# Optimization experiments

Measured on AMD Instinct MI355X. Metric: run time of the kernel, lower is better.

The kernel has to match this reference:

```python
import jax, jax.numpy as jnp
import numpy as np

N, E, F, H, L, G, EMB, C = 50000, 600000, 128, 128, 4, 64, 64, 10
BN_EPS = 1e-5


def setup_inputs() -> dict:
    key = jax.random.key(0)
    k = lambda i: jax.random.fold_in(key, i)
    s = 0.05  # weight scale
    return {
        "x": jax.random.normal(k(0), (N, F), jnp.float32),
        "edge_index": jax.random.randint(k(1), (2, E), 0, N, jnp.int64),
        "batch": jnp.sort(jax.random.randint(k(2), (N,), 0, G, jnp.int64)),
        "emb": jax.random.normal(k(3), (G, EMB), jnp.float32),
        "eps": jnp.zeros((L,), jnp.float32),
        "W1": jax.random.normal(k(4), (L, F, H), jnp.float32) * s,
        "b1": jnp.zeros((L, H), jnp.float32),
        "W2": jax.random.normal(k(5), (L, H, H), jnp.float32) * s,
        "b2": jnp.zeros((L, H), jnp.float32),
        "gamma": jnp.ones((L, H), jnp.float32),
        "beta": jnp.zeros((L, H), jnp.float32),
        "lin1_w": jax.random.normal(k(6), (L * H + EMB, 2 * H), jnp.float32) * s,
        "lin1_b": jnp.zeros((2 * H,), jnp.float32),
        "lin2_w": jax.random.normal(k(7), (2 * H, H), jnp.float32) * s,
        "lin2_b": jnp.zeros((H,), jnp.float32),
        "lin4_w": jax.random.normal(k(8), (H, C), jnp.float32) * s,
        "lin4_b": jnp.zeros((C,), jnp.float32),
    }


def _gin_mlp(h, W1, b1, W2, b2, gamma, beta):
    # Linear -> ReLU -> Linear -> ReLU -> BatchNorm1d (batch stats)
    h = jax.nn.relu(h @ W1 + b1)
    h = jax.nn.relu(h @ W2 + b2)
    mean = jnp.mean(h, axis=0)
    var = jnp.var(h, axis=0)
    return (h - mean) * jax.lax.rsqrt(var + BN_EPS) * gamma + beta


def reference(x, edge_index, batch, emb, eps, W1, b1, W2, b2, gamma, beta,
              lin1_w, lin1_b, lin2_w, lin2_b, lin4_w, lin4_b):
    src, dst = edge_index[0], edge_index[1]
    xs = []
    for l in range(L):
        # GIN: MLP((1+eps)*x_i + sum_{j->i} x_j)  via gather + scatter-add
        agg = jax.ops.segment_sum(x[src], dst, num_segments=N)  # [N,H]
        x = _gin_mlp((1.0 + eps[l]) * x + agg,
                     W1[l], b1[l], W2[l], b2[l], gamma[l], beta[l])
        xs.append(x)
    h = jnp.concatenate(xs, axis=1)  # [N, L*H]
    # global mean pool per graph
    sums = jax.ops.segment_sum(h, batch, num_segments=G)  # [G, L*H]
    cnt = jax.ops.segment_sum(jnp.ones((N,), h.dtype), batch, num_segments=G)
    pooled = sums / jnp.maximum(cnt, 1.0)[:, None]
    z = jnp.concatenate([pooled, emb.reshape(G, -1)], axis=1)
    z = jax.nn.relu(z @ lin1_w + lin1_b)  # .relu() twice is idempotent
    # dropout p=0.5 skipped (eval mode); lin3 unused in original forward
    z = jax.nn.relu(z @ lin2_w + lin2_b)
    z = z @ lin4_w + lin4_b
    return jax.nn.log_softmax(z, axis=1)
```

## Files before the change

### kernel.cpp

```cpp
#include <hip/hip_runtime.h>
#include <cstdint>
#include <cstddef>

#define N_NODES 50000
#define N_EDGES 600000
#define NLAYER  4
#define NGRAPH  64
#define SCAN_NB 196
#define NBLK_MLP ((N_NODES + 127) / 128)
#define CVTX_NB ((N_NODES * 32 + 255) / 256)
#define CVTW_NB ((NLAYER * 128 * 128 * 2) / 256)
#define DEG_NB  ((N_EDGES + 255) / 256)

typedef unsigned int   u32;
typedef unsigned short u16;
typedef unsigned char  u8;
typedef float f32x4  __attribute__((ext_vector_type(4)));
typedef short bf16x8 __attribute__((ext_vector_type(8)));

__device__ __forceinline__ u16 f2bf(float f) {
    u32 x = __float_as_uint(f);
    u32 r = x + 0x7fffu + ((x >> 16) & 1u);
    return (u16)(r >> 16);
}
__device__ __forceinline__ u32 pack2(float a, float b) {
    return (u32)f2bf(a) | ((u32)f2bf(b) << 16);
}

__device__ __forceinline__ float fp8b0(u32 u) { return __builtin_amdgcn_cvt_f32_fp8(u, 0); }
__device__ __forceinline__ float fp8b1(u32 u) { return __builtin_amdgcn_cvt_f32_fp8(u, 1); }
__device__ __forceinline__ u32 pk_fp8(float a, float b) {
    return (u32)__builtin_amdgcn_cvt_pk_fp8_f32(a, b, 0, false);
}

__global__ __launch_bounds__(256) void setup_all(
    const float4* __restrict__ x, u32* __restrict__ xf8,
    const float* __restrict__ W1, const float* __restrict__ W2,
    short* __restrict__ W1t, short* __restrict__ W2t,
    const int* __restrict__ dst, int* __restrict__ deg) {
    int b = blockIdx.x, tid = threadIdx.x;
    if (b < CVTX_NB) {
        int i = b * 256 + tid;
        if (i < N_NODES * 32) {
            float4 v = x[i];
            u32 r = pk_fp8(v.x, v.y);
            r = (u32)__builtin_amdgcn_cvt_pk_fp8_f32(v.z, v.w, (int)r, true);
            xf8[i] = r;
        }
    } else if (b < CVTX_NB + CVTW_NB) {
        int i = (b - CVTX_NB) * 256 + tid;
        int z = i >> 16, r = i & 65535;
        int l = r >> 14, n = (r >> 7) & 127, k = r & 127;
        const float* W = z ? W2 : W1;
        short* Wt      = z ? W2t : W1t;
        Wt[((size_t)l * 128 + n) * 128 + k] = (short)f2bf(W[((size_t)l * 128 + k) * 128 + n]);
    } else {
        int e = (b - CVTX_NB - CVTW_NB) * 256 + tid;
        if (e < N_EDGES) atomicAdd(&deg[dst[e]], 1);
    }
}

__global__ __launch_bounds__(256) void scan_l1(const int* __restrict__ deg,
                                               int* __restrict__ bscan,
                                               int* __restrict__ bsum) {
    __shared__ int sd[256];
    int tid = threadIdx.x;
    int i = blockIdx.x * 256 + tid;
    int v = (i < N_NODES) ? deg[i] : 0;
    sd[tid] = v; __syncthreads();
#pragma unroll
    for (int off = 1; off < 256; off <<= 1) {
        int t = (tid >= off) ? sd[tid - off] : 0;
        __syncthreads();
        sd[tid] += t; __syncthreads();
    }
    if (i < N_NODES) bscan[i] = sd[tid];
    if (tid == 255) bsum[blockIdx.x] = sd[255];
}

__global__ __launch_bounds__(256) void scan_l3(const int* __restrict__ bscan,
                                               const int* __restrict__ bsum,
                                               int* __restrict__ rowp) {
    __shared__ int sd[256];
    __shared__ int sboff;
    int tid = threadIdx.x;
    int v = (tid < SCAN_NB) ? bsum[tid] : 0;
    sd[tid] = v; __syncthreads();
#pragma unroll
    for (int off = 1; off < 256; off <<= 1) {
        int t = (tid >= off) ? sd[tid - off] : 0;
        __syncthreads();
        sd[tid] += t; __syncthreads();
    }
    if (tid == (int)blockIdx.x) sboff = sd[tid] - v;
    __syncthreads();
    int i = blockIdx.x * 256 + tid;
    if (i == 0) rowp[0] = 0;
    if (i < N_NODES) rowp[i + 1] = bscan[i] + sboff;
}

__global__ void fill_csr(const int* __restrict__ src, const int* __restrict__ dst,
                         const int* __restrict__ rowp, int* __restrict__ cursor,
                         int* __restrict__ col) {
    int e = blockIdx.x * 256 + threadIdx.x;
    if (e < N_EDGES) {
        int d = dst[e];
        int pos = atomicAdd(&cursor[d], 1);
        col[rowp[d] + pos] = src[e];
    }
}

__global__ __launch_bounds__(256) void agg_kernel(
    const u16* __restrict__ xin,
    const float* __restrict__ sums_prev,
    const float* __restrict__ gamma, const float* __restrict__ beta,
    int layer, const float* __restrict__ eps_all,
    const int* __restrict__ rowp, const int* __restrict__ col,
    u32* __restrict__ agg) {
    __shared__ float cA[128], cD[128];
    int tid = threadIdx.x;
    if (tid < 128) {
        float a = 1.f, d = 0.f;
        if (sums_prev) {
            float s1 = sums_prev[tid], s2 = sums_prev[128 + tid];
            float mean = s1 * (1.0f / N_NODES);
            float var  = s2 * (1.0f / N_NODES) - mean * mean;
            a = rsqrtf(var + 1e-5f) * gamma[(layer - 1) * 128 + tid];
            d = beta[(layer - 1) * 128 + tid] - mean * a;
        }
        cA[tid] = a; cD[tid] = d;
    }
    __syncthreads();
    int node = blockIdx.x * 4 + (tid >> 6);
    int lane = tid & 63;
    if (node >= N_NODES) return;
    float a0 = cA[2 * lane], a1 = cA[2 * lane + 1];
    float d0 = cD[2 * lane], d1 = cD[2 * lane + 1];
    float ep = 1.0f + eps_all[layer];
    u32 v = xin[(size_t)node * 64 + lane];
    int k0 = rowp[node], k1 = rowp[node + 1];
    float s0 = 0.f, s1 = 0.f;
    int k = k0;
    int cc[8];
    if (k < k1) {
#pragma unroll
        for (int t = 0; t < 8; t++) cc[t] = col[min(k + t, k1 - 1)];
    }
    while (k < k1) {
        int idx[8];
#pragma unroll
        for (int t = 0; t < 8; t++) idx[t] = cc[t];
        int kn = k + 8;
        if (kn < k1) {
#pragma unroll
            for (int t = 0; t < 8; t++) cc[t] = col[min(kn + t, k1 - 1)];
        }
#pragma unroll
        for (int t = 0; t < 8; t++) {
            u32 u = xin[(size_t)idx[t] * 64 + lane];
            float w = (k + t < k1) ? 1.f : 0.f;
            s0 += w * fp8b0(u); s1 += w * fp8b1(u);
        }
        k = kn;
    }
    float deg = (float)(k1 - k0);
    float r0 = ep * (a0 * fp8b0(v) + d0) + a0 * s0 + deg * d0;
    float r1 = ep * (a1 * fp8b1(v) + d1) + a1 * s1 + deg * d1;
    agg[(size_t)node * 64 + lane] = pack2(r0, r1);
}

#define H1_STRIDE 136
__global__ __launch_bounds__(256) void mlp_fused(
    const short* __restrict__ A,
    const short* __restrict__ W1t, const float* __restrict__ b1,
    const short* __restrict__ W2t, const float* __restrict__ b2,
    u8* __restrict__ H2, const int* __restrict__ batch,
    float* __restrict__ sums, float* __restrict__ gsum, int M) {
    __shared__ alignas(16) short h1s[128 * H1_STRIDE];
    __shared__ int sh_ga, sh_gb, sh_split;
    int tid  = threadIdx.x;
    int wave = tid >> 6, lane = tid & 63;
    int ln15 = lane & 15, quad = lane >> 4;
    int m0blk = blockIdx.x * 128;
    int m0 = m0blk + wave * 32;
    const bf16x8 zz = {0, 0, 0, 0, 0, 0, 0, 0};

    if (tid == 0) {
        int rlo = m0blk, rhi = min(m0blk + 127, M - 1);
        int ga = batch[rlo], gb = batch[rhi];
        int split = m0blk + 128;
        if (ga != gb) {
            int lo = rlo, hi = rhi;
            while (lo + 1 < hi) { int mid = (lo + hi) >> 1; if (batch[mid] == ga) lo = mid; else hi = mid; }
            split = hi;
        }
        sh_ga = ga; sh_gb = gb; sh_split = split;
    }

    bf16x8 a[2][4];
#pragma unroll
    for (int rt = 0; rt < 2; rt++) {
        int row = m0 + rt * 16 + ln15;
        const short* rp = A + (size_t)row * 128 + quad * 8;
        bool ok = row < M;
#pragma unroll
        for (int s = 0; s < 4; s++)
            a[rt][s] = ok ? *(const bf16x8*)(rp + s * 32) : zz;
    }
#pragma unroll
    for (int ct = 0; ct < 8; ct++) {
        const short* wp = W1t + (size_t)(ct * 16 + ln15) * 128 + quad * 8;
        bf16x8 b[4];
#pragma unroll
        for (int s = 0; s < 4; s++) b[s] = *(const bf16x8*)(wp + s * 32);
        float bias = b1[ct * 16 + ln15];
#pragma unroll
        for (int rt = 0; rt < 2; rt++) {
            f32x4 acc = {0.f, 0.f, 0.f, 0.f};
#pragma unroll
            for (int s = 0; s < 4; s++)
                acc = __builtin_amdgcn_mfma_f32_16x16x32_bf16(a[rt][s], b[s], acc, 0, 0, 0);
#pragma unroll
            for (int i = 0; i < 4; i++) {
                float v = fmaxf(acc[i] + bias, 0.f);
                int lr = wave * 32 + rt * 16 + quad * 4 + i;
                h1s[lr * H1_STRIDE + ct * 16 + ln15] = (short)f2bf(v);
            }
        }
    }
    __syncthreads();
    bf16x8 c[2][4];
#pragma unroll
    for (int rt = 0; rt < 2; rt++) {
        const short* rp = h1s + (size_t)(wave * 32 + rt * 16 + ln15) * H1_STRIDE + quad * 8;
#pragma unroll
        for (int s = 0; s < 4; s++) c[rt][s] = *(const bf16x8*)(rp + s * 32);
    }
    int gsplit = sh_split;
    float sAcc[8], qAcc[8], pAcc[8];
#pragma unroll
    for (int ct = 0; ct < 8; ct++) { sAcc[ct] = 0.f; qAcc[ct] = 0.f; pAcc[ct] = 0.f; }
#pragma unroll
    for (int ct = 0; ct < 8; ct++) {
        const short* wp = W2t + (size_t)(ct * 16 + ln15) * 128 + quad * 8;
        bf16x8 b[4];
#pragma unroll
        for (int s = 0; s < 4; s++) b[s] = *(const bf16x8*)(wp + s * 32);
        float bias = b2[ct * 16 + ln15];
#pragma unroll
        for (int rt = 0; rt < 2; rt++) {
            f32x4 acc = {0.f, 0.f, 0.f, 0.f};
#pragma unroll
            for (int s = 0; s < 4; s++)
                acc = __builtin_amdgcn_mfma_f32_16x16x32_bf16(c[rt][s], b[s], acc, 0, 0, 0);
            int colx = ct * 16 + ln15;
#pragma unroll
            for (int i = 0; i < 4; i++) {
                int row = m0 + rt * 16 + quad * 4 + i;
                float v = fmaxf(acc[i] + bias, 0.f);
                if (row < M) H2[(size_t)row * 128 + colx] = (u8)(pk_fp8(v, v) & 0xffu);
                float vm = (row < M) ? v : 0.f;
                sAcc[ct] += vm; qAcc[ct] += vm * vm;
                if (row < gsplit) pAcc[ct] += vm;
            }
        }
    }
    __syncthreads();
    float* scr = (float*)h1s;
    int slice = wave * 4 + quad;
#pragma unroll
    for (int ct = 0; ct < 8; ct++) {
        int colx = ct * 16 + ln15;
        scr[(0 * 16 + slice) * 128 + colx] = sAcc[ct];
        scr[(1 * 16 + slice) * 128 + colx] = qAcc[ct];
        scr[(2 * 16 + slice) * 128 + colx] = pAcc[ct];
    }
    __syncthreads();
    if (tid < 128) {
        float ss = 0.f, qq = 0.f, pa = 0.f;
#pragma unroll
        for (int sl = 0; sl < 16; sl++) {
            ss += scr[(0 * 16 + sl) * 128 + tid];
            qq += scr[(1 * 16 + sl) * 128 + tid];
            pa += scr[(2 * 16 + sl) * 128 + tid];
        }
        atomicAdd(&sums[tid], ss);
        atomicAdd(&sums[128 + tid], qq);
        int ga = sh_ga, gb = sh_gb;
        atomicAdd(&gsum[ga * 128 + tid], pa);
        if (gb != ga) atomicAdd(&gsum[gb * 128 + tid], ss - pa);
    }
}

__global__ __launch_bounds__(256) void head_kernel(
    const float* __restrict__ gsum, const float* __restrict__ sumsL,
    const float* __restrict__ gamma, const float* __restrict__ beta,
    const int* __restrict__ batch, const float* __restrict__ emb,
    const float* __restrict__ l1w, const float* __restrict__ l1b,
    const float* __restrict__ l2w, const float* __restrict__ l2b,
    const float* __restrict__ l4w, const float* __restrict__ l4b,
    float* __restrict__ out) {
    __shared__ float z[576];
    __shared__ float z1[256];
    __shared__ float z2h[2][128];
    __shared__ float z2[128];
    __shared__ float zr[128][10];
    __shared__ float inv_cnt;
    int g = blockIdx.x;
    int tid = threadIdx.x;
    if (tid == 0) {
        int lo = 0, hi = N_NODES;
        while (lo < hi) { int m = (lo + hi) >> 1; if (batch[m] < g) lo = m + 1; else hi = m; }
        int s = lo;
        lo = 0; hi = N_NODES;
        while (lo < hi) { int m = (lo + hi) >> 1; if (batch[m] < g + 1) lo = m + 1; else hi = m; }
        inv_cnt = 1.0f / fmaxf((float)(lo - s), 1.0f);
    }
    __syncthreads();
    for (int j = tid; j < 512; j += 256) {
        int l = j >> 7, c = j & 127;
        float s1 = sumsL[l * 256 + c], s2 = sumsL[l * 256 + 128 + c];
        float mean = s1 * (1.0f / N_NODES);
        float var  = s2 * (1.0f / N_NODES) - mean * mean;
        float a = rsqrtf(var + 1e-5f) * gamma[l * 128 + c];
        float d = beta[l * 128 + c] - mean * a;
        z[j] = a * gsum[(size_t)l * NGRAPH * 128 + g * 128 + c] * inv_cnt + d;
    }
    if (tid < 64) z[512 + tid] = emb[g * 64 + tid];
    __syncthreads();
    {
        float acc = l1b[tid];
        for (int j0 = 0; j0 < 576; j0 += 16) {
            float lw[16];
#pragma unroll
            for (int t = 0; t < 16; t++) lw[t] = l1w[(j0 + t) * 256 + tid];
#pragma unroll
            for (int t = 0; t < 16; t++) acc += z[j0 + t] * lw[t];
        }
        z1[tid] = fmaxf(acc, 0.f);
    }
    __syncthreads();
    {
        int c2 = tid & 127, half = tid >> 7;
        float acc = 0.f;
        int jb = half * 128;
        for (int j0 = 0; j0 < 128; j0 += 8) {
            float lw[8];
#pragma unroll
            for (int t = 0; t < 8; t++) lw[t] = l2w[(jb + j0 + t) * 128 + c2];
#pragma unroll
            for (int t = 0; t < 8; t++) acc += z1[jb + j0 + t] * lw[t];
        }
        z2h[half][c2] = acc;
    }
    __syncthreads();
    if (tid < 128) z2[tid] = fmaxf(z2h[0][tid] + z2h[1][tid] + l2b[tid], 0.f);
    __syncthreads();
    if (tid < 128) {
        float zv = z2[tid];
        const float* wr = l4w + tid * 10;
#pragma unroll
        for (int c = 0; c < 10; c++) zr[tid][c] = zv * wr[c];
    }
    __syncthreads();
    for (int s = 64; s >= 1; s >>= 1) {
        if (tid < s) {
#pragma unroll
            for (int c = 0; c < 10; c++) zr[tid][c] += zr[tid + s][c];
        }
        __syncthreads();
    }
    if (tid == 0) {
        float z3s[10];
#pragma unroll
        for (int c = 0; c < 10; c++) z3s[c] = zr[0][c] + l4b[c];
        float m = z3s[0];
        for (int i = 1; i < 10; i++) m = fmaxf(m, z3s[i]);
        float se = 0.f;
        for (int i = 0; i < 10; i++) se += expf(z3s[i] - m);
        float lse = m + logf(se);
        for (int i = 0; i < 10; i++) out[g * 10 + i] = z3s[i] - lse;
    }
}

extern "C" void kernel_launch(void* const* d_in, const int* in_sizes, int n_in,
                              void* d_out, int out_size, void* d_ws, size_t ws_size,
                              hipStream_t stream) {
    (void)in_sizes; (void)n_in; (void)out_size; (void)ws_size;
    const float* x0   = (const float*)d_in[0];
    const int* ei     = (const int*)d_in[1];
    const int* src    = ei;
    const int* dst    = ei + N_EDGES;
    const int* batch  = (const int*)d_in[2];
    const float* emb  = (const float*)d_in[3];
    const float* eps  = (const float*)d_in[4];
    const float* W1   = (const float*)d_in[5];
    const float* b1   = (const float*)d_in[6];
    const float* W2   = (const float*)d_in[7];
    const float* b2   = (const float*)d_in[8];
    const float* gamma= (const float*)d_in[9];
    const float* beta = (const float*)d_in[10];
    const float* l1w  = (const float*)d_in[11];
    const float* l1b  = (const float*)d_in[12];
    const float* l2w  = (const float*)d_in[13];
    const float* l2b  = (const float*)d_in[14];
    const float* l4w  = (const float*)d_in[15];
    const float* l4b  = (const float*)d_in[16];

    char* ws = (char*)d_ws;
    size_t off = 0;
    auto alloc = [&](size_t bytes) -> char* {
        char* p = ws + off; off += (bytes + 255) & ~(size_t)255; return p;
    };
    int* deg    = (int*)alloc(N_NODES * 4);
    int* cursor = (int*)alloc(N_NODES * 4);
    float* sumsL = (float*)alloc(NLAYER * 256 * 4);
    float* gsumL = (float*)alloc((size_t)NLAYER * NGRAPH * 128 * 4);
    size_t zero_len = (char*)gsumL - (char*)deg + (size_t)NLAYER * NGRAPH * 128 * 4;
    int* rowp   = (int*)alloc((N_NODES + 1) * 4);
    int* bscan  = (int*)alloc(N_NODES * 4);
    int* bsum   = (int*)alloc(SCAN_NB * 4);
    int* col    = (int*)alloc(N_EDGES * 4);
    u8* xf8     = (u8*)alloc((size_t)N_NODES * 128);
    u8* h2a     = (u8*)alloc((size_t)N_NODES * 128);
    u8* h2b     = (u8*)alloc((size_t)N_NODES * 128);
    u32* agg    = (u32*)alloc((size_t)N_NODES * 64 * 4);
    short* W1t  = (short*)alloc((size_t)NLAYER * 128 * 128 * 2);
    short* W2t  = (short*)alloc((size_t)NLAYER * 128 * 128 * 2);

    hipMemsetAsync(deg, 0, zero_len, stream);

    setup_all<<<CVTX_NB + CVTW_NB + DEG_NB, 256, 0, stream>>>(
        (const float4*)x0, (u32*)xf8, W1, W2, W1t, W2t, dst, deg);
    scan_l1<<<SCAN_NB, 256, 0, stream>>>(deg, bscan, bsum);
    scan_l3<<<SCAN_NB, 256, 0, stream>>>(bscan, bsum, rowp);
    fill_csr<<<(N_EDGES + 255) / 256, 256, 0, stream>>>(src, dst, rowp, cursor, col);

    const u8* xin = xf8;
    for (int l = 0; l < NLAYER; ++l) {
        u8* h2 = (l & 1) ? h2b : h2a;
        const float* sums_prev = (l == 0) ? nullptr : (sumsL + (l - 1) * 256);
        agg_kernel<<<(N_NODES + 3) / 4, 256, 0, stream>>>(
            (const u16*)xin, sums_prev, gamma, beta, l, eps, rowp, col, agg);
        mlp_fused<<<NBLK_MLP, 256, 0, stream>>>(
            (const short*)agg, W1t + (size_t)l * 16384, b1 + l * 128,
            W2t + (size_t)l * 16384, b2 + l * 128, h2, batch,
            sumsL + l * 256, gsumL + (size_t)l * NGRAPH * 128, N_NODES);
        xin = h2;
    }
    head_kernel<<<NGRAPH, 256, 0, stream>>>(gsumL, sumsL, gamma, beta, batch, emb,
                                            l1w, l1b, l2w, l2b, l4w, l4b,
                                            (float*)d_out);
}
```

Baseline: 408.9 us.

## Halve MLP rows per block and reuse degree-atomic ranks in CSR fill

The fused MLP kernel now processes 64 rows per block, one 16-row tile per wave, instead of 128. This halves LDS and register use per block and doubles the block count, with a shuffle-based reduction of column statistics before the shared-memory pass. The CSR build keeps the return value of the degree atomic as each edge's rank, so fill_csr no longer needs a second atomic pass over a cursor array. The cost is an extra edge-sized rank buffer and twice as many global atomics for the per-block statistics.

```diff
diff --git a/kernel.cpp b/kernel.cpp
--- a/kernel.cpp
+++ b/kernel.cpp
@@ -7,7 +7,8 @@
 #define NLAYER  4
 #define NGRAPH  64
 #define SCAN_NB 196
-#define NBLK_MLP ((N_NODES + 127) / 128)
+#define MROWS   64
+#define NBLK_MLP ((N_NODES + MROWS - 1) / MROWS)
 #define CVTX_NB ((N_NODES * 32 + 255) / 256)
 #define CVTW_NB ((NLAYER * 128 * 128 * 2) / 256)
 #define DEG_NB  ((N_EDGES + 255) / 256)
@@ -37,7 +38,8 @@
     const float4* __restrict__ x, u32* __restrict__ xf8,
     const float* __restrict__ W1, const float* __restrict__ W2,
     short* __restrict__ W1t, short* __restrict__ W2t,
-    const int* __restrict__ dst, int* __restrict__ deg) {
+    const int* __restrict__ dst, int* __restrict__ deg,
+    int* __restrict__ rank) {
     int b = blockIdx.x, tid = threadIdx.x;
     if (b < CVTX_NB) {
         int i = b * 256 + tid;
@@ -56,7 +58,7 @@
         Wt[((size_t)l * 128 + n) * 128 + k] = (short)f2bf(W[((size_t)l * 128 + k) * 128 + n]);
     } else {
         int e = (b - CVTX_NB - CVTW_NB) * 256 + tid;
-        if (e < N_EDGES) atomicAdd(&deg[dst[e]], 1);
+        if (e < N_EDGES) rank[e] = atomicAdd(&deg[dst[e]], 1);
     }
 }
 
@@ -99,15 +101,12 @@
     if (i < N_NODES) rowp[i + 1] = bscan[i] + sboff;
 }
 
-__global__ void fill_csr(const int* __restrict__ src, const int* __restrict__ dst,
-                         const int* __restrict__ rowp, int* __restrict__ cursor,
-                         int* __restrict__ col) {
+__global__ __launch_bounds__(256) void fill_csr(
+    const int* __restrict__ src, const int* __restrict__ dst,
+    const int* __restrict__ rowp, const int* __restrict__ rank,
+    int* __restrict__ col) {
     int e = blockIdx.x * 256 + threadIdx.x;
-    if (e < N_EDGES) {
-        int d = dst[e];
-        int pos = atomicAdd(&cursor[d], 1);
-        col[rowp[d] + pos] = src[e];
-    }
+    if (e < N_EDGES) col[rowp[dst[e]] + rank[e]] = src[e];
 }
 
 __global__ __launch_bounds__(256) void agg_kernel(
@@ -169,26 +168,27 @@
     agg[(size_t)node * 64 + lane] = pack2(r0, r1);
 }
 
-#define H1_STRIDE 136
+#define H1_STR 136
 __global__ __launch_bounds__(256) void mlp_fused(
     const short* __restrict__ A,
     const short* __restrict__ W1t, const float* __restrict__ b1,
     const short* __restrict__ W2t, const float* __restrict__ b2,
     u8* __restrict__ H2, const int* __restrict__ batch,
     float* __restrict__ sums, float* __restrict__ gsum, int M) {
-    __shared__ alignas(16) short h1s[128 * H1_STRIDE];
+    __shared__ alignas(16) short h1s[MROWS * H1_STR];
+    __shared__ float scr[3 * 4 * 128];
     __shared__ int sh_ga, sh_gb, sh_split;
     int tid  = threadIdx.x;
     int wave = tid >> 6, lane = tid & 63;
     int ln15 = lane & 15, quad = lane >> 4;
-    int m0blk = blockIdx.x * 128;
-    int m0 = m0blk + wave * 32;
+    int m0blk = blockIdx.x * MROWS;
+    int row0 = m0blk + wave * 16;
     const bf16x8 zz = {0, 0, 0, 0, 0, 0, 0, 0};
 
     if (tid == 0) {
-        int rlo = m0blk, rhi = min(m0blk + 127, M - 1);
+        int rlo = m0blk, rhi = min(m0blk + MROWS - 1, M - 1);
         int ga = batch[rlo], gb = batch[rhi];
-        int split = m0blk + 128;
+        int split = m0blk + MROWS;
         if (ga != gb) {
             int lo = rlo, hi = rhi;
             while (lo + 1 < hi) { int mid = (lo + hi) >> 1; if (batch[mid] == ga) lo = mid; else hi = mid; }
@@ -197,15 +197,14 @@
         sh_ga = ga; sh_gb = gb; sh_split = split;
     }
 
-    bf16x8 a[2][4];
-#pragma unroll
-    for (int rt = 0; rt < 2; rt++) {
-        int row = m0 + rt * 16 + ln15;
+    bf16x8 a[4];
+    {
+        int row = row0 + ln15;
         const short* rp = A + (size_t)row * 128 + quad * 8;
         bool ok = row < M;
 #pragma unroll
         for (int s = 0; s < 4; s++)
-            a[rt][s] = ok ? *(const bf16x8*)(rp + s * 32) : zz;
+            a[s] = ok ? *(const bf16x8*)(rp + s * 32) : zz;
     }
 #pragma unroll
     for (int ct = 0; ct < 8; ct++) {
@@ -214,28 +213,23 @@
 #pragma unroll
         for (int s = 0; s < 4; s++) b[s] = *(const bf16x8*)(wp + s * 32);
         float bias = b1[ct * 16 + ln15];
-#pragma unroll
-        for (int rt = 0; rt < 2; rt++) {
-            f32x4 acc = {0.f, 0.f, 0.f, 0.f};
-#pragma unroll
-            for (int s = 0; s < 4; s++)
-                acc = __builtin_amdgcn_mfma_f32_16x16x32_bf16(a[rt][s], b[s], acc, 0, 0, 0);
-#pragma unroll
-            for (int i = 0; i < 4; i++) {
-                float v = fmaxf(acc[i] + bias, 0.f);
-                int lr = wave * 32 + rt * 16 + quad * 4 + i;
-                h1s[lr * H1_STRIDE + ct * 16 + ln15] = (short)f2bf(v);
-            }
-        }
-    }
-    __syncthreads();
-    bf16x8 c[2][4];
-#pragma unroll
-    for (int rt = 0; rt < 2; rt++) {
-        const short* rp = h1s + (size_t)(wave * 32 + rt * 16 + ln15) * H1_STRIDE + quad * 8;
-#pragma unroll
-        for (int s = 0; s < 4; s++) c[rt][s] = *(const bf16x8*)(rp + s * 32);
-    }
+        f32x4 acc = {0.f, 0.f, 0.f, 0.f};
+#pragma unroll
+        for (int s = 0; s < 4; s++)
+            acc = __builtin_amdgcn_mfma_f32_16x16x32_bf16(a[s], b[s], acc, 0, 0, 0);
+#pragma unroll
+        for (int i = 0; i < 4; i++) {
+            float v = fmaxf(acc[i] + bias, 0.f);
+            int lr = wave * 16 + quad * 4 + i;
+            h1s[lr * H1_STR + ct * 16 + ln15] = (short)f2bf(v);
+        }
+    }
+    __syncthreads();
+    bf16x8 c[4];
+#pragma unroll
+    for (int s = 0; s < 4; s++)
+        c[s] = *(const bf16x8*)&h1s[(wave * 16 + ln15) * H1_STR + quad * 8 + s * 32];
+
     int gsplit = sh_split;
     float sAcc[8], qAcc[8], pAcc[8];
 #pragma unroll
@@ -247,42 +241,44 @@
 #pragma unroll
         for (int s = 0; s < 4; s++) b[s] = *(const bf16x8*)(wp + s * 32);
         float bias = b2[ct * 16 + ln15];
-#pragma unroll
-        for (int rt = 0; rt < 2; rt++) {
-            f32x4 acc = {0.f, 0.f, 0.f, 0.f};
-#pragma unroll
-            for (int s = 0; s < 4; s++)
-                acc = __builtin_amdgcn_mfma_f32_16x16x32_bf16(c[rt][s], b[s], acc, 0, 0, 0);
+        f32x4 acc = {0.f, 0.f, 0.f, 0.f};
+#pragma unroll
+        for (int s = 0; s < 4; s++)
+            acc = __builtin_amdgcn_mfma_f32_16x16x32_bf16(c[s], b[s], acc, 0, 0, 0);
+        int colx = ct * 16 + ln15;
+#pragma unroll
+        for (int i = 0; i < 4; i++) {
+            int row = row0 + quad * 4 + i;
+            float v = fmaxf(acc[i] + bias, 0.f);
+            if (row < M) H2[(size_t)row * 128 + colx] = (u8)(pk_fp8(v, v) & 0xffu);
+            float vm = (row < M) ? v : 0.f;
+            sAcc[ct] += vm; qAcc[ct] += vm * vm;
+            if (row < gsplit) pAcc[ct] += vm;
+        }
+    }
+#pragma unroll
+    for (int ct = 0; ct < 8; ct++) {
+        sAcc[ct] += __shfl_xor(sAcc[ct], 16); sAcc[ct] += __shfl_xor(sAcc[ct], 32);
+        qAcc[ct] += __shfl_xor(qAcc[ct], 16); qAcc[ct] += __shfl_xor(qAcc[ct], 32);
+        pAcc[ct] += __shfl_xor(pAcc[ct], 16); pAcc[ct] += __shfl_xor(pAcc[ct], 32);
+    }
+    if (quad == 0) {
+#pragma unroll
+        for (int ct = 0; ct < 8; ct++) {
             int colx = ct * 16 + ln15;
-#pragma unroll
-            for (int i = 0; i < 4; i++) {
-                int row = m0 + rt * 16 + quad * 4 + i;
-                float v = fmaxf(acc[i] + bias, 0.f);
-                if (row < M) H2[(size_t)row * 128 + colx] = (u8)(pk_fp8(v, v) & 0xffu);
-                float vm = (row < M) ? v : 0.f;
-                sAcc[ct] += vm; qAcc[ct] += vm * vm;
-                if (row < gsplit) pAcc[ct] += vm;
-            }
-        }
-    }
-    __syncthreads();
-    float* scr = (float*)h1s;
-    int slice = wave * 4 + quad;
-#pragma unroll
-    for (int ct = 0; ct < 8; ct++) {
-        int colx = ct * 16 + ln15;
-        scr[(0 * 16 + slice) * 128 + colx] = sAcc[ct];
-        scr[(1 * 16 + slice) * 128 + colx] = qAcc[ct];
-        scr[(2 * 16 + slice) * 128 + colx] = pAcc[ct];
+            scr[(0 * 4 + wave) * 128 + colx] = sAcc[ct];
+            scr[(1 * 4 + wave) * 128 + colx] = qAcc[ct];
+            scr[(2 * 4 + wave) * 128 + colx] = pAcc[ct];
+        }
     }
     __syncthreads();
     if (tid < 128) {
         float ss = 0.f, qq = 0.f, pa = 0.f;
 #pragma unroll
-        for (int sl = 0; sl < 16; sl++) {
-            ss += scr[(0 * 16 + sl) * 128 + tid];
-            qq += scr[(1 * 16 + sl) * 128 + tid];
-            pa += scr[(2 * 16 + sl) * 128 + tid];
+        for (int w = 0; w < 4; w++) {
+            ss += scr[(0 * 4 + w) * 128 + tid];
+            qq += scr[(1 * 4 + w) * 128 + tid];
+            pa += scr[(2 * 4 + w) * 128 + tid];
         }
         atomicAdd(&sums[tid], ss);
         atomicAdd(&sums[128 + tid], qq);
@@ -413,7 +409,6 @@
         char* p = ws + off; off += (bytes + 255) & ~(size_t)255; return p;
     };
     int* deg    = (int*)alloc(N_NODES * 4);
-    int* cursor = (int*)alloc(N_NODES * 4);
     float* sumsL = (float*)alloc(NLAYER * 256 * 4);
     float* gsumL = (float*)alloc((size_t)NLAYER * NGRAPH * 128 * 4);
     size_t zero_len = (char*)gsumL - (char*)deg + (size_t)NLAYER * NGRAPH * 128 * 4;
@@ -421,6 +416,7 @@
     int* bscan  = (int*)alloc(N_NODES * 4);
     int* bsum   = (int*)alloc(SCAN_NB * 4);
     int* col    = (int*)alloc(N_EDGES * 4);
+    int* rank   = (int*)alloc(N_EDGES * 4);
     u8* xf8     = (u8*)alloc((size_t)N_NODES * 128);
     u8* h2a     = (u8*)alloc((size_t)N_NODES * 128);
     u8* h2b     = (u8*)alloc((size_t)N_NODES * 128);
@@ -431,10 +427,10 @@
     hipMemsetAsync(deg, 0, zero_len, stream);
 
     setup_all<<<CVTX_NB + CVTW_NB + DEG_NB, 256, 0, stream>>>(
-        (const float4*)x0, (u32*)xf8, W1, W2, W1t, W2t, dst, deg);
+        (const float4*)x0, (u32*)xf8, W1, W2, W1t, W2t, dst, deg, rank);
     scan_l1<<<SCAN_NB, 256, 0, stream>>>(deg, bscan, bsum);
     scan_l3<<<SCAN_NB, 256, 0, stream>>>(bscan, bsum, rowp);
-    fill_csr<<<(N_EDGES + 255) / 256, 256, 0, stream>>>(src, dst, rowp, cursor, col);
+    fill_csr<<<(N_EDGES + 255) / 256, 256, 0, stream>>>(src, dst, rowp, rank, col);
 
     const u8* xin = xf8;
     for (int l = 0; l < NLAYER; ++l) {
```

Result: slower. 458.7 us (+12.2%).

## Fuse neighbor aggregation and GIN MLP into one per-layer 16-node kernel

Applied to the files above, without the earlier changes.

Replaces the separate aggregation kernel and MLP kernel with a single 1024-thread kernel per layer. Each block gathers 16 nodes into LDS, then waves 0-7 compute the first GEMM and waves 8-15 the second, which removes the bf16 agg round trip through global memory and one launch per layer. BatchNorm statistics are spread across 8 replicated sum buffers to reduce atomic contention, which the consumers now sum back together. The cost is a much larger grid with small MFMA tiles, weights reloaded per 16-node block, and half the waves idle during each GEMM phase.

```diff
diff --git a/kernel.cpp b/kernel.cpp
--- a/kernel.cpp
+++ b/kernel.cpp
@@ -7,7 +7,8 @@
 #define NLAYER  4
 #define NGRAPH  64
 #define SCAN_NB 196
-#define NBLK_MLP ((N_NODES + 127) / 128)
+#define LNODES  16
+#define LF_NB   (N_NODES / LNODES)
 #define CVTX_NB ((N_NODES * 32 + 255) / 256)
 #define CVTW_NB ((NLAYER * 128 * 128 * 2) / 256)
 #define DEG_NB  ((N_EDGES + 255) / 256)
@@ -110,19 +111,35 @@
     }
 }
 
-__global__ __launch_bounds__(256) void agg_kernel(
+#define AST 136
+__global__ __launch_bounds__(1024, 8) void layer16(
     const u16* __restrict__ xin,
     const float* __restrict__ sums_prev,
     const float* __restrict__ gamma, const float* __restrict__ beta,
     int layer, const float* __restrict__ eps_all,
     const int* __restrict__ rowp, const int* __restrict__ col,
-    u32* __restrict__ agg) {
+    const short* __restrict__ W1t, const float* __restrict__ b1,
+    const short* __restrict__ W2t, const float* __restrict__ b2,
+    u8* __restrict__ H2, const int* __restrict__ batch,
+    float* __restrict__ sums8, float* __restrict__ gsum, int M) {
     __shared__ float cA[128], cD[128];
-    int tid = threadIdx.x;
+    __shared__ alignas(16) short As[LNODES * AST];
+    __shared__ alignas(16) short h1s[LNODES * AST];
+    __shared__ int sh_ga, sh_gb, sh_split;
+    int tid  = threadIdx.x;
+    int wave = tid >> 6, lane = tid & 63;
+    int ln15 = lane & 15, quad = lane >> 4;
+    int m0 = blockIdx.x * LNODES;
+
     if (tid < 128) {
         float a = 1.f, d = 0.f;
         if (sums_prev) {
-            float s1 = sums_prev[tid], s2 = sums_prev[128 + tid];
+            float s1 = 0.f, s2 = 0.f;
+#pragma unroll
+            for (int b = 0; b < 8; b++) {
+                s1 += sums_prev[b * 256 + tid];
+                s2 += sums_prev[b * 256 + 128 + tid];
+            }
             float mean = s1 * (1.0f / N_NODES);
             float var  = s2 * (1.0f / N_NODES) - mean * mean;
             a = rsqrtf(var + 1e-5f) * gamma[(layer - 1) * 128 + tid];
@@ -130,65 +147,10 @@
         }
         cA[tid] = a; cD[tid] = d;
     }
-    __syncthreads();
-    int node = blockIdx.x * 4 + (tid >> 6);
-    int lane = tid & 63;
-    if (node >= N_NODES) return;
-    float a0 = cA[2 * lane], a1 = cA[2 * lane + 1];
-    float d0 = cD[2 * lane], d1 = cD[2 * lane + 1];
-    float ep = 1.0f + eps_all[layer];
-    u32 v = xin[(size_t)node * 64 + lane];
-    int k0 = rowp[node], k1 = rowp[node + 1];
-    float s0 = 0.f, s1 = 0.f;
-    int k = k0;
-    int cc[8];
-    if (k < k1) {
-#pragma unroll
-        for (int t = 0; t < 8; t++) cc[t] = col[min(k + t, k1 - 1)];
-    }
-    while (k < k1) {
-        int idx[8];
-#pragma unroll
-        for (int t = 0; t < 8; t++) idx[t] = cc[t];
-        int kn = k + 8;
-        if (kn < k1) {
-#pragma unroll
-            for (int t = 0; t < 8; t++) cc[t] = col[min(kn + t, k1 - 1)];
-        }
-#pragma unroll
-        for (int t = 0; t < 8; t++) {
-            u32 u = xin[(size_t)idx[t] * 64 + lane];
-            float w = (k + t < k1) ? 1.f : 0.f;
-            s0 += w * fp8b0(u); s1 += w * fp8b1(u);
-        }
-        k = kn;
-    }
-    float deg = (float)(k1 - k0);
-    float r0 = ep * (a0 * fp8b0(v) + d0) + a0 * s0 + deg * d0;
-    float r1 = ep * (a1 * fp8b1(v) + d1) + a1 * s1 + deg * d1;
-    agg[(size_t)node * 64 + lane] = pack2(r0, r1);
-}
-
-#define H1_STRIDE 136
-__global__ __launch_bounds__(256) void mlp_fused(
-    const short* __restrict__ A,
-    const short* __restrict__ W1t, const float* __restrict__ b1,
-    const short* __restrict__ W2t, const float* __restrict__ b2,
-    u8* __restrict__ H2, const int* __restrict__ batch,
-    float* __restrict__ sums, float* __restrict__ gsum, int M) {
-    __shared__ alignas(16) short h1s[128 * H1_STRIDE];
-    __shared__ int sh_ga, sh_gb, sh_split;
-    int tid  = threadIdx.x;
-    int wave = tid >> 6, lane = tid & 63;
-    int ln15 = lane & 15, quad = lane >> 4;
-    int m0blk = blockIdx.x * 128;
-    int m0 = m0blk + wave * 32;
-    const bf16x8 zz = {0, 0, 0, 0, 0, 0, 0, 0};
-
     if (tid == 0) {
-        int rlo = m0blk, rhi = min(m0blk + 127, M - 1);
+        int rlo = m0, rhi = min(m0 + LNODES - 1, M - 1);
         int ga = batch[rlo], gb = batch[rhi];
-        int split = m0blk + 128;
+        int split = m0 + LNODES;
         if (ga != gb) {
             int lo = rlo, hi = rhi;
             while (lo + 1 < hi) { int mid = (lo + hi) >> 1; if (batch[mid] == ga) lo = mid; else hi = mid; }
@@ -196,99 +158,106 @@
         }
         sh_ga = ga; sh_gb = gb; sh_split = split;
     }
-
-    bf16x8 a[2][4];
-#pragma unroll
-    for (int rt = 0; rt < 2; rt++) {
-        int row = m0 + rt * 16 + ln15;
-        const short* rp = A + (size_t)row * 128 + quad * 8;
-        bool ok = row < M;
+    __syncthreads();
+
+    {
+        int node = m0 + wave;
+        float a0 = cA[2 * lane], a1 = cA[2 * lane + 1];
+        float d0 = cD[2 * lane], d1 = cD[2 * lane + 1];
+        float ep = 1.0f + eps_all[layer];
+        u32 v = xin[(size_t)node * 64 + lane];
+        int k0 = rowp[node], k1 = rowp[node + 1];
+        float s0 = 0.f, s1 = 0.f;
+        int k = k0;
+        int cc[8];
+        if (k < k1) {
+#pragma unroll
+            for (int t = 0; t < 8; t++) cc[t] = col[min(k + t, k1 - 1)];
+        }
+        while (k < k1) {
+            int idx[8];
+#pragma unroll
+            for (int t = 0; t < 8; t++) idx[t] = cc[t];
+            int kn = k + 8;
+            if (kn < k1) {
+#pragma unroll
+                for (int t = 0; t < 8; t++) cc[t] = col[min(kn + t, k1 - 1)];
+            }
+#pragma unroll
+            for (int t = 0; t < 8; t++) {
+                u32 u = xin[(size_t)idx[t] * 64 + lane];
+                float w = (k + t < k1) ? 1.f : 0.f;
+                s0 += w * fp8b0(u); s1 += w * fp8b1(u);
+            }
+            k = kn;
+        }
+        float deg = (float)(k1 - k0);
+        float r0 = ep * (a0 * fp8b0(v) + d0) + a0 * s0 + deg * d0;
+        float r1 = ep * (a1 * fp8b1(v) + d1) + a1 * s1 + deg * d1;
+        *(u32*)&As[wave * AST + 2 * lane] = pack2(r0, r1);
+    }
+    __syncthreads();
+
+    bf16x8 w2b[4];
+    if (wave >= 8) {
+        const short* wp = W2t + (size_t)((wave - 8) * 16 + ln15) * 128 + quad * 8;
+#pragma unroll
+        for (int s = 0; s < 4; s++) w2b[s] = *(const bf16x8*)(wp + s * 32);
+    } else {
+        int ct = wave;
+        const short* wp = W1t + (size_t)(ct * 16 + ln15) * 128 + quad * 8;
+        bf16x8 a[4], b[4];
+#pragma unroll
+        for (int s = 0; s < 4; s++) b[s] = *(const bf16x8*)(wp + s * 32);
 #pragma unroll
         for (int s = 0; s < 4; s++)
-            a[rt][s] = ok ? *(const bf16x8*)(rp + s * 32) : zz;
-    }
-#pragma unroll
-    for (int ct = 0; ct < 8; ct++) {
-        const short* wp = W1t + (size_t)(ct * 16 + ln15) * 128 + quad * 8;
-        bf16x8 b[4];
-#pragma unroll
-        for (int s = 0; s < 4; s++) b[s] = *(const bf16x8*)(wp + s * 32);
+            a[s] = *(const bf16x8*)&As[ln15 * AST + quad * 8 + s * 32];
         float bias = b1[ct * 16 + ln15];
-#pragma unroll
-        for (int rt = 0; rt < 2; rt++) {
-            f32x4 acc = {0.f, 0.f, 0.f, 0.f};
-#pragma unroll
-            for (int s = 0; s < 4; s++)
-                acc = __builtin_amdgcn_mfma_f32_16x16x32_bf16(a[rt][s], b[s], acc, 0, 0, 0);
-#pragma unroll
-            for (int i = 0; i < 4; i++) {
-                float v = fmaxf(acc[i] + bias, 0.f);
-                int lr = wave * 32 + rt * 16 + quad * 4 + i;
-                h1s[lr * H1_STRIDE + ct * 16 + ln15] = (short)f2bf(v);
-            }
-        }
-    }
-    __syncthreads();
-    bf16x8 c[2][4];
-#pragma unroll
-    for (int rt = 0; rt < 2; rt++) {
-        const short* rp = h1s + (size_t)(wave * 32 + rt * 16 + ln15) * H1_STRIDE + quad * 8;
-#pragma unroll
-        for (int s = 0; s < 4; s++) c[rt][s] = *(const bf16x8*)(rp + s * 32);
-    }
-    int gsplit = sh_split;
-    float sAcc[8], qAcc[8], pAcc[8];
-#pragma unroll
-    for (int ct = 0; ct < 8; ct++) { sAcc[ct] = 0.f; qAcc[ct] = 0.f; pAcc[ct] = 0.f; }
-#pragma unroll
-    for (int ct = 0; ct < 8; ct++) {
-        const short* wp = W2t + (size_t)(ct * 16 + ln15) * 128 + quad * 8;
-        bf16x8 b[4];
-#pragma unroll
-        for (int s = 0; s < 4; s++) b[s] = *(const bf16x8*)(wp + s * 32);
+        f32x4 acc = {0.f, 0.f, 0.f, 0.f};
+#pragma unroll
+        for (int s = 0; s < 4; s++)
+            acc = __builtin_amdgcn_mfma_f32_16x16x32_bf16(a[s], b[s], acc, 0, 0, 0);
+#pragma unroll
+        for (int i = 0; i < 4; i++) {
+            float v = fmaxf(acc[i] + bias, 0.f);
+            h1s[(quad * 4 + i) * AST + ct * 16 + ln15] = (short)f2bf(v);
+        }
+    }
+    __syncthreads();
+
+    if (wave >= 8) {
+        int ct = wave - 8;
+        bf16x8 c[4];
+#pragma unroll
+        for (int s = 0; s < 4; s++)
+            c[s] = *(const bf16x8*)&h1s[ln15 * AST + quad * 8 + s * 32];
         float bias = b2[ct * 16 + ln15];
-#pragma unroll
-        for (int rt = 0; rt < 2; rt++) {
-            f32x4 acc = {0.f, 0.f, 0.f, 0.f};
-#pragma unroll
-            for (int s = 0; s < 4; s++)
-                acc = __builtin_amdgcn_mfma_f32_16x16x32_bf16(c[rt][s], b[s], acc, 0, 0, 0);
-            int colx = ct * 16 + ln15;
-#pragma unroll
-            for (int i = 0; i < 4; i++) {
-                int row = m0 + rt * 16 + quad * 4 + i;
-                float v = fmaxf(acc[i] + bias, 0.f);
-                if (row < M) H2[(size_t)row * 128 + colx] = (u8)(pk_fp8(v, v) & 0xffu);
-                float vm = (row < M) ? v : 0.f;
-                sAcc[ct] += vm; qAcc[ct] += vm * vm;
-                if (row < gsplit) pAcc[ct] += vm;
-            }
-        }
-    }
-    __syncthreads();
-    float* scr = (float*)h1s;
-    int slice = wave * 4 + quad;
-#pragma unroll
-    for (int ct = 0; ct < 8; ct++) {
+        f32x4 acc = {0.f, 0.f, 0.f, 0.f};
+#pragma unroll
+        for (int s = 0; s < 4; s++)
+            acc = __builtin_amdgcn_mfma_f32_16x16x32_bf16(c[s], w2b[s], acc, 0, 0, 0);
         int colx = ct * 16 + ln15;
-        scr[(0 * 16 + slice) * 128 + colx] = sAcc[ct];
-        scr[(1 * 16 + slice) * 128 + colx] = qAcc[ct];
-        scr[(2 * 16 + slice) * 128 + colx] = pAcc[ct];
-    }
-    __syncthreads();
-    if (tid < 128) {
-        float ss = 0.f, qq = 0.f, pa = 0.f;
-#pragma unroll
-        for (int sl = 0; sl < 16; sl++) {
-            ss += scr[(0 * 16 + sl) * 128 + tid];
-            qq += scr[(1 * 16 + sl) * 128 + tid];
-            pa += scr[(2 * 16 + sl) * 128 + tid];
-        }
-        atomicAdd(&sums[tid], ss);
-        atomicAdd(&sums[128 + tid], qq);
-        int ga = sh_ga, gb = sh_gb;
-        atomicAdd(&gsum[ga * 128 + tid], pa);
-        if (gb != ga) atomicAdd(&gsum[gb * 128 + tid], ss - pa);
+        int gsplit = sh_split;
+        float sA = 0.f, qA = 0.f, pA = 0.f;
+#pragma unroll
+        for (int i = 0; i < 4; i++) {
+            int row = m0 + quad * 4 + i;
+            float v = fmaxf(acc[i] + bias, 0.f);
+            H2[(size_t)row * 128 + colx] = (u8)(pk_fp8(v, v) & 0xffu);
+            sA += v; qA += v * v;
+            if (row < gsplit) pA += v;
+        }
+        sA += __shfl_xor(sA, 16); sA += __shfl_xor(sA, 32);
+        qA += __shfl_xor(qA, 16); qA += __shfl_xor(qA, 32);
+        pA += __shfl_xor(pA, 16); pA += __shfl_xor(pA, 32);
+        if (quad == 0) {
+            float* sb = sums8 + (size_t)(blockIdx.x & 7) * 256;
+            atomicAdd(&sb[colx], sA);
+            atomicAdd(&sb[128 + colx], qA);
+            int ga = sh_ga, gb = sh_gb;
+            atomicAdd(&gsum[ga * 128 + colx], pA);
+            if (gb != ga) atomicAdd(&gsum[gb * 128 + colx], sA - pA);
+        }
     }
 }
 
@@ -319,7 +288,12 @@
     __syncthreads();
     for (int j = tid; j < 512; j += 256) {
         int l = j >> 7, c = j & 127;
-        float s1 = sumsL[l * 256 + c], s2 = sumsL[l * 256 + 128 + c];
+        float s1 = 0.f, s2 = 0.f;
+#pragma unroll
+        for (int b = 0; b < 8; b++) {
+            s1 += sumsL[(size_t)l * 2048 + b * 256 + c];
+            s2 += sumsL[(size_t)l * 2048 + b * 256 + 128 + c];
+        }
         float mean = s1 * (1.0f / N_NODES);
         float var  = s2 * (1.0f / N_NODES) - mean * mean;
         float a = rsqrtf(var + 1e-5f) * gamma[l * 128 + c];
@@ -414,7 +388,7 @@
     };
     int* deg    = (int*)alloc(N_NODES * 4);
     int* cursor = (int*)alloc(N_NODES * 4);
-    float* sumsL = (float*)alloc(NLAYER * 256 * 4);
+    float* sumsL = (float*)alloc((size_t)NLAYER * 8 * 256 * 4);
     float* gsumL = (float*)alloc((size_t)NLAYER * NGRAPH * 128 * 4);
     size_t zero_len = (char*)gsumL - (char*)deg + (size_t)NLAYER * NGRAPH * 128 * 4;
     int* rowp   = (int*)alloc((N_NODES + 1) * 4);
@@ -424,7 +398,6 @@
     u8* xf8     = (u8*)alloc((size_t)N_NODES * 128);
     u8* h2a     = (u8*)alloc((size_t)N_NODES * 128);
     u8* h2b     = (u8*)alloc((size_t)N_NODES * 128);
-    u32* agg    = (u32*)alloc((size_t)N_NODES * 64 * 4);
     short* W1t  = (short*)alloc((size_t)NLAYER * 128 * 128 * 2);
     short* W2t  = (short*)alloc((size_t)NLAYER * 128 * 128 * 2);
 
@@ -439,13 +412,13 @@
     const u8* xin = xf8;
     for (int l = 0; l < NLAYER; ++l) {
         u8* h2 = (l & 1) ? h2b : h2a;
-        const float* sums_prev = (l == 0) ? nullptr : (sumsL + (l - 1) * 256);
-        agg_kernel<<<(N_NODES + 3) / 4, 256, 0, stream>>>(
-            (const u16*)xin, sums_prev, gamma, beta, l, eps, rowp, col, agg);
-        mlp_fused<<<NBLK_MLP, 256, 0, stream>>>(
-            (const short*)agg, W1t + (size_t)l * 16384, b1 + l * 128,
-            W2t + (size_t)l * 16384, b2 + l * 128, h2, batch,
-            sumsL + l * 256, gsumL + (size_t)l * NGRAPH * 128, N_NODES);
+        const float* sums_prev = (l == 0) ? nullptr : (sumsL + (size_t)(l - 1) * 2048);
+        layer16<<<LF_NB, 1024, 0, stream>>>(
+            (const u16*)xin, sums_prev, gamma, beta, l, eps, rowp, col,
+            W1t + (size_t)l * 16384, b1 + l * 128,
+            W2t + (size_t)l * 16384, b2 + l * 128,
+            h2, batch, sumsL + (size_t)l * 2048,
+            gsumL + (size_t)l * NGRAPH * 128, N_NODES);
         xin = h2;
     }
     head_kernel<<<NGRAPH, 256, 0, stream>>>(gsumL, sumsL, gamma, beta, batch, emb,
```

New measurement: 418.4 us. 1.02x slower.
